# Kernel optimization log

Measured on AMD Instinct MI355X. Metric: run time of the kernel, lower is better.

## Reference

```python
import jax, jax.numpy as jnp
import numpy as np

TOP_K = 2

def setup_inputs() -> dict:
    key = jax.random.key(0)
    k1, k2 = jax.random.split(key)
    D, E = 4096, 64
    hidden_states = jax.random.normal(k1, (2, 8192, D), dtype=jnp.float32)
    W = jax.random.normal(k2, (E, D), dtype=jnp.float32) / np.sqrt(D)
    b = jnp.zeros((E,), dtype=jnp.float32)
    return {"hidden_states": hidden_states, "W": W, "b": b}

def reference(hidden_states, W, b):
    # gate: logits [B, S, E]
    logits = jnp.einsum('bsd,ed->bse', hidden_states, W) + b
    scores = jax.nn.softmax(logits, axis=-1)
    top_k_values, top_k_indices = jax.lax.top_k(scores, TOP_K)
    return ((top_k_indices, top_k_values), scores)
```

## Files before the change

kernel.cpp:

```cpp
#include <hip/hip_runtime.h>
#include <math.h>

#define D_DIM 4096
#define E_DIM 64
#define TM 64
#define KSPLIT 4
#define KPART (D_DIM / KSPLIT)
#define CHK 64
#define NCH (KPART / CHK)
#define WROW 72
#define WSCALE 1024.0f
#define ISCALE (1.0f / 1024.0f)

typedef __attribute__((ext_vector_type(8))) __fp16 f16x8;
typedef __attribute__((ext_vector_type(2))) __fp16 f16x2;
typedef __attribute__((ext_vector_type(4))) float f32x4;

__device__ inline void split2(const f32x4 a0, const f32x4 a1, f16x8& fh, f16x8& fl) {
    float f[8] = {a0[0], a0[1], a0[2], a0[3], a1[0], a1[1], a1[2], a1[3]};
    union { f16x8 v; f16x2 p[4]; } H, L;
    #pragma unroll
    for (int j = 0; j < 4; ++j) {
        const f16x2 h = __builtin_amdgcn_cvt_pkrtz(f[2*j], f[2*j+1]);
        const float r0 = f[2*j]     - (float)h[0];
        const float r1 = f[2*j + 1] - (float)h[1];
        H.p[j] = h;
        L.p[j] = __builtin_amdgcn_cvt_pkrtz(r0, r1);
    }
    fh = H.v; fl = L.v;
}

__global__ __launch_bounds__(256, 4) void router_gemm(
    const float* __restrict__ hs,
    const float* __restrict__ W,
    float* __restrict__ logits,
    int nTok)
{
    __shared__ __fp16 wsh[2][E_DIM * WROW];
    __shared__ __fp16 wsl[2][E_DIM * WROW];

    const int tid  = threadIdx.x;
    const int lane = tid & 63;
    const int wv   = tid >> 6;
    const int part = blockIdx.x & (KSPLIT - 1);
    const int tb   = (blockIdx.x >> 2) * TM;
    const int kb   = part * KPART;

    const int l15 = lane & 15;
    const int lq  = lane >> 4;

    const float* aptr = hs + (size_t)(tb + wv * 16 + l15) * D_DIM + kb + lq * 8;
    const int we = tid >> 2;
    const int wq = tid & 3;
    const float* wptr = W + (size_t)we * D_DIM + kb + wq * 16;

    f32x4 acc[4];
    #pragma unroll
    for (int t = 0; t < 4; ++t) acc[t] = (f32x4){0.f, 0.f, 0.f, 0.f};

    f32x4 ca[4], pa[4], wr[4];

    auto loadA = [&](int ch, f32x4* dst) {
        const float* p = aptr + ch * CHK;
        dst[0] = *(const f32x4*)(p);
        dst[1] = *(const f32x4*)(p + 4);
        dst[2] = *(const f32x4*)(p + 32);
        dst[3] = *(const f32x4*)(p + 36);
    };
    auto loadW = [&](int ch) {
        const float* p = wptr + ch * CHK;
        wr[0] = *(const f32x4*)(p);
        wr[1] = *(const f32x4*)(p + 4);
        wr[2] = *(const f32x4*)(p + 8);
        wr[3] = *(const f32x4*)(p + 12);
    };
    auto storeW = [&](int buf) {
        f16x8 h0, l0, h1, l1;
        split2(wr[0] * WSCALE, wr[1] * WSCALE, h0, l0);
        split2(wr[2] * WSCALE, wr[3] * WSCALE, h1, l1);
        const int base = we * WROW + wq * 16;
        *(f16x8*)&wsh[buf][base] = h0;  *(f16x8*)&wsh[buf][base + 8] = h1;
        *(f16x8*)&wsl[buf][base] = l0;  *(f16x8*)&wsl[buf][base + 8] = l1;
    };
    auto compute = [&](const f32x4* a, int buf) {
        #pragma unroll
        for (int s = 0; s < 2; ++s) {
            f16x8 ah, al;
            split2(a[2 * s], a[2 * s + 1], ah, al);
            const int koff = s * 32 + lq * 8;
            #pragma unroll
            for (int t = 0; t < 4; ++t) {
                const int rb = (t * 16 + l15) * WROW + koff;
                const f16x8 bh = *(const f16x8*)&wsh[buf][rb];
                const f16x8 bl = *(const f16x8*)&wsl[buf][rb];
                acc[t] = __builtin_amdgcn_mfma_f32_16x16x32_f16(ah, bh, acc[t], 0, 0, 0);
                acc[t] = __builtin_amdgcn_mfma_f32_16x16x32_f16(ah, bl, acc[t], 0, 0, 0);
                acc[t] = __builtin_amdgcn_mfma_f32_16x16x32_f16(al, bh, acc[t], 0, 0, 0);
            }
        }
    };

    loadA(0, ca);
    loadW(0);
    storeW(0);
    __syncthreads();
    int buf = 0;
    #pragma unroll 1
    for (int ch = 0; ch < NCH; ++ch) {
        const bool last = (ch == NCH - 1);
        if (!last) {
            loadA(ch + 1, pa);
            loadW(ch + 1);
        }
        compute(ca, buf);
        if (!last) {
            storeW(buf ^ 1);
            __syncthreads();
            #pragma unroll
            for (int i = 0; i < 4; ++i) ca[i] = pa[i];
            buf ^= 1;
        }
    }

    float* dst = logits + (size_t)(tb + wv * 16) * E_DIM;
    #pragma unroll
    for (int t = 0; t < 4; ++t)
        #pragma unroll
        for (int r = 0; r < 4; ++r)
            unsafeAtomicAdd(&dst[(size_t)(lq * 4 + r) * E_DIM + t * 16 + l15], acc[t][r] * ISCALE);
}

__global__ __launch_bounds__(256, 4) void router_epilogue(
    const float* __restrict__ bias,
    float* __restrict__ out,
    int nTok)
{
    const int tid = threadIdx.x;
    const int tok = blockIdx.x * 64 + (tid >> 2);
    const int g   = tid & 3;

    float* out_idx = out;
    float* out_val = out + (size_t)nTok * 2;
    float* sc      = out + (size_t)nTok * 4;

    float* src = sc + (size_t)tok * E_DIM + g * 16;
    float v[16];
    #pragma unroll
    for (int j = 0; j < 4; ++j) {
        const f32x4 x = *(const f32x4*)(src + j * 4);
        const f32x4 b = *(const f32x4*)(bias + g * 16 + j * 4);
        v[j * 4 + 0] = x[0] + b[0];
        v[j * 4 + 1] = x[1] + b[1];
        v[j * 4 + 2] = x[2] + b[2];
        v[j * 4 + 3] = x[3] + b[3];
    }

    float b1 = -INFINITY, b2 = -INFINITY;
    int i1 = 0, i2 = 0;
    #pragma unroll
    for (int j = 0; j < 16; ++j) {
        const float x = v[j];
        const int idx = g * 16 + j;
        if (x > b1)      { b2 = b1; i2 = i1; b1 = x; i1 = idx; }
        else if (x > b2) { b2 = x; i2 = idx; }
    }
    #pragma unroll
    for (int d = 1; d <= 2; d <<= 1) {
        const float ob1 = __shfl_xor(b1, d);
        const int   oi1 = __shfl_xor(i1, d);
        const float ob2 = __shfl_xor(b2, d);
        const int   oi2 = __shfl_xor(i2, d);
        if (ob1 > b1 || (ob1 == b1 && oi1 < i1)) {
            if (b1 > ob2 || (b1 == ob2 && i1 < oi2)) { b2 = b1; i2 = i1; }
            else                                     { b2 = ob2; i2 = oi2; }
            b1 = ob1; i1 = oi1;
        } else {
            if (ob1 > b2 || (ob1 == b2 && oi1 < i2)) { b2 = ob1; i2 = oi1; }
        }
    }
    const float m = b1;

    float e[16];
    float s = 0.f;
    #pragma unroll
    for (int j = 0; j < 16; ++j) { e[j] = __expf(v[j] - m); s += e[j]; }
    s += __shfl_xor(s, 1);
    s += __shfl_xor(s, 2);
    const float inv = 1.f / s;

    if (g == 0) {
        out_idx[(size_t)tok * 2 + 0] = (float)i1;
        out_idx[(size_t)tok * 2 + 1] = (float)i2;
        out_val[(size_t)tok * 2 + 0] = inv;
        out_val[(size_t)tok * 2 + 1] = __expf(b2 - m) * inv;
    }

    #pragma unroll
    for (int j = 0; j < 4; ++j) {
        f32x4 o;
        o[0] = e[j * 4 + 0] * inv;
        o[1] = e[j * 4 + 1] * inv;
        o[2] = e[j * 4 + 2] * inv;
        o[3] = e[j * 4 + 3] * inv;
        *(f32x4*)(src + j * 4) = o;
    }
}

extern "C" void kernel_launch(void* const* d_in, const int* in_sizes, int n_in,
                              void* d_out, int out_size, void* d_ws, size_t ws_size,
                              hipStream_t stream) {
    const float* hs = (const float*)d_in[0];
    const float* W  = (const float*)d_in[1];
    const float* b  = (const float*)d_in[2];
    float* out = (float*)d_out;
    const int nTok = in_sizes[0] / D_DIM;

    float* logits = out + (size_t)nTok * 4;
    hipMemsetAsync(logits, 0, (size_t)nTok * E_DIM * sizeof(float), stream);

    dim3 g1(nTok / TM * KSPLIT), b1(256);
    router_gemm<<<g1, b1, 0, stream>>>(hs, W, logits, nTok);

    dim3 g2(nTok / 64), b2(256);
    router_epilogue<<<g2, b2, 0, stream>>>(b, out, nTok);
}
```

Baseline: 382.8 us.

## Fuse router GEMM with softmax/top-k epilogue and drop K-split atomics

Replaces the split-K GEMM with global atomics plus a separate epilogue kernel with one fused kernel. Each 512-thread block owns 32 tokens over the full K. Logits are staged in LDS and the softmax and top-2 are done in place, removing the memset, the atomic adds and the logits round trip through global memory. W tiles now use a single XOR-swizzled LDS buffer with 128-wide chunks. The cost is that each block re-reads and re-splits all of W to fp16 hi/lo, with fewer blocks and more W traffic per token.

```diff
diff --git a/kernel.cpp b/kernel.cpp
--- a/kernel.cpp
+++ b/kernel.cpp
@@ -3,12 +3,11 @@
 
 #define D_DIM 4096
 #define E_DIM 64
-#define TM 64
-#define KSPLIT 4
-#define KPART (D_DIM / KSPLIT)
-#define CHK 64
-#define NCH (KPART / CHK)
-#define WROW 72
+#define TM 32
+#define CHK 128
+#define NCH (D_DIM / CHK)
+#define HC 16384
+#define SROW 68
 #define WSCALE 1024.0f
 #define ISCALE (1.0f / 1024.0f)
 
@@ -30,42 +29,45 @@
     fh = H.v; fl = L.v;
 }
 
-__global__ __launch_bounds__(256, 4) void router_gemm(
+__global__ __launch_bounds__(512, 4) void router_fused(
     const float* __restrict__ hs,
     const float* __restrict__ W,
-    float* __restrict__ logits,
+    const float* __restrict__ bias,
+    float* __restrict__ out,
     int nTok)
 {
-    __shared__ __fp16 wsh[2][E_DIM * WROW];
-    __shared__ __fp16 wsl[2][E_DIM * WROW];
+    __shared__ __attribute__((aligned(16))) __fp16 wbuf[2][HC];
 
     const int tid  = threadIdx.x;
     const int lane = tid & 63;
     const int wv   = tid >> 6;
-    const int part = blockIdx.x & (KSPLIT - 1);
-    const int tb   = (blockIdx.x >> 2) * TM;
-    const int kb   = part * KPART;
-
-    const int l15 = lane & 15;
-    const int lq  = lane >> 4;
-
-    const float* aptr = hs + (size_t)(tb + wv * 16 + l15) * D_DIM + kb + lq * 8;
-    const int we = tid >> 2;
-    const int wq = tid & 3;
-    const float* wptr = W + (size_t)we * D_DIM + kb + wq * 16;
-
-    f32x4 acc[4];
-    #pragma unroll
-    for (int t = 0; t < 4; ++t) acc[t] = (f32x4){0.f, 0.f, 0.f, 0.f};
-
-    f32x4 ca[4], pa[4], wr[4];
+    const int th   = wv >> 2;
+    const int eq   = wv & 3;
+    const int l15  = lane & 15;
+    const int lq   = lane >> 4;
+    const int tb   = blockIdx.x * TM;
+
+    const float* aptr = hs + (size_t)(tb + th * 16 + l15) * D_DIM + lq * 8;
+    const int erow = (eq * 16 + l15) * 128;
+    const int g0   = lq ^ (l15 & 7);
+
+    const int we = tid >> 3;
+    const int wa = tid & 7;
+    const float* wptr = W + (size_t)we * D_DIM + wa * 16;
+    const int wbase = we * 128;
+    const int gp0 = ((2 * wa)     ^ (we & 7)) * 8;
+    const int gp1 = ((2 * wa + 1) ^ (we & 7)) * 8;
+
+    f32x4 acc = (f32x4){0.f, 0.f, 0.f, 0.f};
+    f32x4 ca[8], pa[8], wr[4];
 
     auto loadA = [&](int ch, f32x4* dst) {
         const float* p = aptr + ch * CHK;
-        dst[0] = *(const f32x4*)(p);
-        dst[1] = *(const f32x4*)(p + 4);
-        dst[2] = *(const f32x4*)(p + 32);
-        dst[3] = *(const f32x4*)(p + 36);
+        #pragma unroll
+        for (int s = 0; s < 4; ++s) {
+            dst[2*s]     = *(const f32x4*)(p + s * 32);
+            dst[2*s + 1] = *(const f32x4*)(p + s * 32 + 4);
+        }
     };
     auto loadW = [&](int ch) {
         const float* p = wptr + ch * CHK;
@@ -78,25 +80,21 @@
         f16x8 h0, l0, h1, l1;
         split2(wr[0] * WSCALE, wr[1] * WSCALE, h0, l0);
         split2(wr[2] * WSCALE, wr[3] * WSCALE, h1, l1);
-        const int base = we * WROW + wq * 16;
-        *(f16x8*)&wsh[buf][base] = h0;  *(f16x8*)&wsh[buf][base + 8] = h1;
-        *(f16x8*)&wsl[buf][base] = l0;  *(f16x8*)&wsl[buf][base + 8] = l1;
+        __fp16* b = &wbuf[buf][0];
+        *(f16x8*)&b[wbase + gp0]        = h0;  *(f16x8*)&b[wbase + gp1]        = h1;
+        *(f16x8*)&b[8192 + wbase + gp0] = l0;  *(f16x8*)&b[8192 + wbase + gp1] = l1;
     };
     auto compute = [&](const f32x4* a, int buf) {
         #pragma unroll
-        for (int s = 0; s < 2; ++s) {
+        for (int s = 0; s < 4; ++s) {
             f16x8 ah, al;
-            split2(a[2 * s], a[2 * s + 1], ah, al);
-            const int koff = s * 32 + lq * 8;
-            #pragma unroll
-            for (int t = 0; t < 4; ++t) {
-                const int rb = (t * 16 + l15) * WROW + koff;
-                const f16x8 bh = *(const f16x8*)&wsh[buf][rb];
-                const f16x8 bl = *(const f16x8*)&wsl[buf][rb];
-                acc[t] = __builtin_amdgcn_mfma_f32_16x16x32_f16(ah, bh, acc[t], 0, 0, 0);
-                acc[t] = __builtin_amdgcn_mfma_f32_16x16x32_f16(ah, bl, acc[t], 0, 0, 0);
-                acc[t] = __builtin_amdgcn_mfma_f32_16x16x32_f16(al, bh, acc[t], 0, 0, 0);
-            }
+            split2(a[2*s], a[2*s + 1], ah, al);
+            const int go = (g0 ^ (s << 2)) * 8;
+            const f16x8 bh = *(const f16x8*)&wbuf[buf][erow + go];
+            const f16x8 bl = *(const f16x8*)&wbuf[buf][8192 + erow + go];
+            acc = __builtin_amdgcn_mfma_f32_16x16x32_f16(ah, bh, acc, 0, 0, 0);
+            acc = __builtin_amdgcn_mfma_f32_16x16x32_f16(ah, bl, acc, 0, 0, 0);
+            acc = __builtin_amdgcn_mfma_f32_16x16x32_f16(al, bh, acc, 0, 0, 0);
         }
     };
 
@@ -113,96 +111,95 @@
             loadW(ch + 1);
         }
         compute(ca, buf);
+        if (!last) storeW(buf ^ 1);
+        __syncthreads();
         if (!last) {
-            storeW(buf ^ 1);
-            __syncthreads();
             #pragma unroll
-            for (int i = 0; i < 4; ++i) ca[i] = pa[i];
-            buf ^= 1;
-        }
-    }
-
-    float* dst = logits + (size_t)(tb + wv * 16) * E_DIM;
-    #pragma unroll
-    for (int t = 0; t < 4; ++t)
+            for (int i = 0; i < 8; ++i) ca[i] = pa[i];
+        }
+        buf ^= 1;
+    }
+
+    float* sc_lds = (float*)&wbuf[0][0];
+    {
+        const int e = eq * 16 + l15;
         #pragma unroll
         for (int r = 0; r < 4; ++r)
-            unsafeAtomicAdd(&dst[(size_t)(lq * 4 + r) * E_DIM + t * 16 + l15], acc[t][r] * ISCALE);
-}
-
-__global__ __launch_bounds__(256, 4) void router_epilogue(
-    const float* __restrict__ bias,
-    float* __restrict__ out,
-    int nTok)
-{
-    const int tid = threadIdx.x;
-    const int tok = blockIdx.x * 64 + (tid >> 2);
-    const int g   = tid & 3;
-
-    float* out_idx = out;
-    float* out_val = out + (size_t)nTok * 2;
-    float* sc      = out + (size_t)nTok * 4;
-
-    float* src = sc + (size_t)tok * E_DIM + g * 16;
-    float v[16];
-    #pragma unroll
-    for (int j = 0; j < 4; ++j) {
-        const f32x4 x = *(const f32x4*)(src + j * 4);
-        const f32x4 b = *(const f32x4*)(bias + g * 16 + j * 4);
-        v[j * 4 + 0] = x[0] + b[0];
-        v[j * 4 + 1] = x[1] + b[1];
-        v[j * 4 + 2] = x[2] + b[2];
-        v[j * 4 + 3] = x[3] + b[3];
-    }
-
-    float b1 = -INFINITY, b2 = -INFINITY;
-    int i1 = 0, i2 = 0;
-    #pragma unroll
-    for (int j = 0; j < 16; ++j) {
-        const float x = v[j];
-        const int idx = g * 16 + j;
-        if (x > b1)      { b2 = b1; i2 = i1; b1 = x; i1 = idx; }
-        else if (x > b2) { b2 = x; i2 = idx; }
-    }
-    #pragma unroll
-    for (int d = 1; d <= 2; d <<= 1) {
-        const float ob1 = __shfl_xor(b1, d);
-        const int   oi1 = __shfl_xor(i1, d);
-        const float ob2 = __shfl_xor(b2, d);
-        const int   oi2 = __shfl_xor(i2, d);
-        if (ob1 > b1 || (ob1 == b1 && oi1 < i1)) {
-            if (b1 > ob2 || (b1 == ob2 && i1 < oi2)) { b2 = b1; i2 = i1; }
-            else                                     { b2 = ob2; i2 = oi2; }
-            b1 = ob1; i1 = oi1;
-        } else {
-            if (ob1 > b2 || (ob1 == b2 && oi1 < i2)) { b2 = ob1; i2 = oi1; }
-        }
-    }
-    const float m = b1;
-
-    float e[16];
-    float s = 0.f;
-    #pragma unroll
-    for (int j = 0; j < 16; ++j) { e[j] = __expf(v[j] - m); s += e[j]; }
-    s += __shfl_xor(s, 1);
-    s += __shfl_xor(s, 2);
-    const float inv = 1.f / s;
-
-    if (g == 0) {
-        out_idx[(size_t)tok * 2 + 0] = (float)i1;
-        out_idx[(size_t)tok * 2 + 1] = (float)i2;
-        out_val[(size_t)tok * 2 + 0] = inv;
-        out_val[(size_t)tok * 2 + 1] = __expf(b2 - m) * inv;
-    }
-
-    #pragma unroll
-    for (int j = 0; j < 4; ++j) {
-        f32x4 o;
-        o[0] = e[j * 4 + 0] * inv;
-        o[1] = e[j * 4 + 1] * inv;
-        o[2] = e[j * 4 + 2] * inv;
-        o[3] = e[j * 4 + 3] * inv;
-        *(f32x4*)(src + j * 4) = o;
+            sc_lds[(th * 16 + lq * 4 + r) * SROW + e] = acc[r] * ISCALE;
+    }
+    __syncthreads();
+
+    if (tid < TM * 4) {
+        const int token = tid >> 2;
+        const int g     = tid & 3;
+        const int gtok  = tb + token;
+
+        float* out_idx = out;
+        float* out_val = out + (size_t)nTok * 2;
+        float* sc      = out + (size_t)nTok * 4;
+
+        const float* srcl = sc_lds + token * SROW + g * 16;
+        float v[16];
+        #pragma unroll
+        for (int j = 0; j < 4; ++j) {
+            const f32x4 x = *(const f32x4*)(srcl + j * 4);
+            const f32x4 b = *(const f32x4*)(bias + g * 16 + j * 4);
+            v[j*4 + 0] = x[0] + b[0];
+            v[j*4 + 1] = x[1] + b[1];
+            v[j*4 + 2] = x[2] + b[2];
+            v[j*4 + 3] = x[3] + b[3];
+        }
+
+        float b1 = -INFINITY, b2 = -INFINITY;
+        int i1 = 0, i2 = 0;
+        #pragma unroll
+        for (int j = 0; j < 16; ++j) {
+            const float x = v[j];
+            const int idx = g * 16 + j;
+            if (x > b1)      { b2 = b1; i2 = i1; b1 = x; i1 = idx; }
+            else if (x > b2) { b2 = x; i2 = idx; }
+        }
+        #pragma unroll
+        for (int d = 1; d <= 2; d <<= 1) {
+            const float ob1 = __shfl_xor(b1, d);
+            const int   oi1 = __shfl_xor(i1, d);
+            const float ob2 = __shfl_xor(b2, d);
+            const int   oi2 = __shfl_xor(i2, d);
+            if (ob1 > b1 || (ob1 == b1 && oi1 < i1)) {
+                if (b1 > ob2 || (b1 == ob2 && i1 < oi2)) { b2 = b1; i2 = i1; }
+                else                                     { b2 = ob2; i2 = oi2; }
+                b1 = ob1; i1 = oi1;
+            } else {
+                if (ob1 > b2 || (ob1 == b2 && oi1 < i2)) { b2 = ob1; i2 = oi1; }
+            }
+        }
+        const float m = b1;
+
+        float e[16];
+        float s = 0.f;
+        #pragma unroll
+        for (int j = 0; j < 16; ++j) { e[j] = __expf(v[j] - m); s += e[j]; }
+        s += __shfl_xor(s, 1);
+        s += __shfl_xor(s, 2);
+        const float inv = 1.f / s;
+
+        if (g == 0) {
+            out_idx[(size_t)gtok * 2 + 0] = (float)i1;
+            out_idx[(size_t)gtok * 2 + 1] = (float)i2;
+            out_val[(size_t)gtok * 2 + 0] = inv;
+            out_val[(size_t)gtok * 2 + 1] = __expf(b2 - m) * inv;
+        }
+
+        float* dstg = sc + (size_t)gtok * E_DIM + g * 16;
+        #pragma unroll
+        for (int j = 0; j < 4; ++j) {
+            f32x4 o;
+            o[0] = e[j*4 + 0] * inv;
+            o[1] = e[j*4 + 1] * inv;
+            o[2] = e[j*4 + 2] * inv;
+            o[3] = e[j*4 + 3] * inv;
+            *(f32x4*)(dstg + j * 4) = o;
+        }
     }
 }
 
@@ -215,12 +212,5 @@
     float* out = (float*)d_out;
     const int nTok = in_sizes[0] / D_DIM;
 
-    float* logits = out + (size_t)nTok * 4;
-    hipMemsetAsync(logits, 0, (size_t)nTok * E_DIM * sizeof(float), stream);
-
-    dim3 g1(nTok / TM * KSPLIT), b1(256);
-    router_gemm<<<g1, b1, 0, stream>>>(hs, W, logits, nTok);
-
-    dim3 g2(nTok / 64), b2(256);
-    router_epilogue<<<g2, b2, 0, stream>>>(b, out, nTok);
+    router_fused<<<dim3(nTok / TM), dim3(512), 0, stream>>>(hs, W, b, out, nTok);
 }
```

Result: slower. 443.6 us (+15.9%).
